# Kernel tuning notes

Hardware: AMD Instinct MI355X
Metric: run time of the kernel (lower is better)

## Reference

```python
import jax, jax.numpy as jnp
import numpy as np

B, H, P, D, NF = 16, 16, 128, 128, 12  # patches == head_dim required by lin_qk


def setup_inputs() -> dict:
    key = jax.random.key(0)
    ks = jax.random.split(key, 8)
    return {
        "q": jax.random.normal(ks[0], (B, H, P, D), jnp.float32),
        "k": jax.random.normal(ks[1], (B, H, P, D), jnp.float32),
        "scale": jnp.ones((1,), jnp.float32),  # unused by the original forward
        "grid": jnp.arange(NF, dtype=jnp.float32) + 1.0,
        "base_weight": jax.random.uniform(ks[2], (D, D), jnp.float32),
        "coef_q": jax.random.uniform(ks[3], (D, NF), jnp.float32),
        "coef_k": jax.random.uniform(ks[4], (D, NF), jnp.float32),
        "scale_base": jnp.ones((1, H, P, D), jnp.float32),
        "scale_sp": jnp.ones((1, H, P, D), jnp.float32),
        "w_qk": jax.random.normal(ks[5], (D, D), jnp.float32) / np.float32(np.sqrt(D)),
        "b_qk": jnp.zeros((D,), jnp.float32),
    }


def _branch(x, coef, grid, base_weight, scale_sp, scale_base):
    # base path: SiLU(x) @ W^T  (F.linear semantics)
    base = jax.nn.silu(x) @ base_weight.T
    # KAN sin basis: sin(grid_f * x_d) -> (B,H,P,NF,D); contract coef[d,f]
    s = jnp.sin(grid[:, None] * x[..., None, :])
    f = jnp.einsum('df,bhpfd->bhpd', coef, s)
    return jax.nn.sigmoid(f * scale_sp + base * scale_base)


def reference(q, k, scale, grid, base_weight, coef_q, coef_k, scale_base, scale_sp, w_qk, b_qk):
    # Per-channel sigmoids, then sum over D. The original builds the full
    # (B,H,P,P,D) broadcast tensor sig_q[...,p,None,:] + sig_k[...,None,p',:]
    # and sums over D; that is exactly separable:
    #   sum_d(sig_q[p,d]) + sum_d(sig_k[p',d])
    sq = _branch(q, coef_q, grid, base_weight, scale_sp, scale_base).sum(-1)  # (B,H,P)
    sk = _branch(k, coef_k, grid, base_weight, scale_sp, scale_base).sum(-1)  # (B,H,P)
    f_out = sq[..., :, None] + sk[..., None, :]  # (B,H,P,P)
    f_out = f_out @ w_qk.T + b_qk  # lin_qk: valid because patches == head_dim
    return jax.nn.softmax(f_out, axis=-1)
```

## Files before the change

kernel.cpp:

```cpp
#include <hip/hip_runtime.h>
#include <hip/hip_bf16.h>


typedef float          f32x4 __attribute__((ext_vector_type(4)));
typedef short          s16x8 __attribute__((ext_vector_type(8)));
typedef int            s32x4 __attribute__((ext_vector_type(4)));
typedef unsigned short u16x8 __attribute__((ext_vector_type(8)));

#define LOG2E   1.44269504f
#define NLOG2E -1.44269504f
#define INV2PI  0.15915494309189535f

static __device__ __forceinline__ float hw_exp2(float x) {
    float r;
    asm("v_exp_f32 %0, %1" : "=v"(r) : "v"(x));
    return r;
}
static __device__ __forceinline__ float hw_fract(float x) {
    float r;
    asm("v_fract_f32 %0, %1" : "=v"(r) : "v"(x));
    return r;
}
static __device__ __forceinline__ float hw_sin01(float f) {
    float r;
    asm("v_sin_f32 %0, %1" : "=v"(r) : "v"(f));
    return r;
}
static __device__ __forceinline__ float hw_cos01(float f) {
    float r;
    asm("v_cos_f32 %0, %1" : "=v"(r) : "v"(f));
    return r;
}
static __device__ __forceinline__ float fastrcp(float x) {
    return __builtin_amdgcn_rcpf(x);
}
static __device__ __forceinline__ unsigned int cvt_pk_bf16(float lo, float hi) {
    unsigned int r;
    asm("v_cvt_pk_bf16_f32 %0, %1, %2" : "=v"(r) : "v"(lo), "v"(hi));
    return r;
}
static __device__ __forceinline__ float sigmoid_fast(float z) {
    return fastrcp(1.f + hw_exp2(z * NLOG2E));
}
static __device__ __forceinline__ int swz(int local) {
    return local ^ (((local >> 8) & 7) << 4);
}

__global__ __launch_bounds__(256) void k_convert(const float* __restrict__ bw,
                                                 unsigned short* __restrict__ wbf) {
    int i = blockIdx.x * 256 + threadIdx.x;
    if (i < 128 * 128) {
        __hip_bfloat16 h = __float2bfloat16(bw[i]);
        unsigned short r;
        __builtin_memcpy(&r, &h, 2);
        wbf[i] = r;
    }
}

__global__ __launch_bounds__(512, 4) void k_branch(
    const float* __restrict__ q, const float* __restrict__ k,
    const unsigned short* __restrict__ wbf,
    const float* __restrict__ gridv,
    const float* __restrict__ coef_q, const float* __restrict__ coef_k,
    const float* __restrict__ sbase,
    const float* __restrict__ ssp,
    float* __restrict__ sums_lo, float* __restrict__ sums_hi)
{
    __shared__ char smem[32768 + 6144];
    float* cfl = (float*)(smem + 32768);

    const int t = threadIdx.x;
    const int lane = t & 63, w = t >> 6;
    const int wr = w >> 1;
    const int ch = w & 1;
    const int r15 = lane & 15, g4 = lane >> 4;
    const int row0 = blockIdx.x * 64;
    const bool is_q = row0 < 32768;
    const float* X = is_q ? q : k;
    const float* coef = is_q ? coef_q : coef_k;
    const int xrow0 = is_q ? row0 : row0 - 32768;
    const float g1 = gridv[0];
    const float grev = g1 * INV2PI;

    #pragma unroll
    for (int it = 0; it < 4; ++it) {
        int c = it * 512 + t;
        u16x8 v = *(const u16x8*)&wbf[c * 8];
        *(u16x8*)(smem + swz(c * 16)) = v;
    }
    #pragma unroll
    for (int it = 0; it < 3; ++it) {
        int e = it * 512 + t;
        float v = coef[e];
        int d = e / 12, u = e - d * 12;
        cfl[u * 128 + d] = v;
    }
    __syncthreads();

    const int xrow = wr * 16 + r15;
    const float* xrowp = &X[(xrow0 + xrow) * 128];
    const int hp = (row0 + xrow) & 2047;
    const float* ssprow = &ssp[hp * 128];

    f32x4 acc[4];
    #pragma unroll
    for (int n = 0; n < 4; ++n) acc[n] = (f32x4){0.f, 0.f, 0.f, 0.f};
    float fv[16];

    #pragma unroll
    for (int s = 0; s < 4; ++s) {
        const float4* xp = (const float4*)&xrowp[s * 32 + g4 * 8];
        float4 x0 = xp[0], x1 = xp[1];
        float xsv[8] = {x0.x, x0.y, x0.z, x0.w, x1.x, x1.y, x1.z, x1.w};
        float sl[8];
        #pragma unroll
        for (int j = 0; j < 8; ++j) {
            float e = hw_exp2(xsv[j] * NLOG2E);
            sl[j] = xsv[j] * fastrcp(1.f + e);
        }
        s32x4 a4 = {(int)cvt_pk_bf16(sl[0], sl[1]), (int)cvt_pk_bf16(sl[2], sl[3]),
                    (int)cvt_pk_bf16(sl[4], sl[5]), (int)cvt_pk_bf16(sl[6], sl[7])};
        s16x8 af = __builtin_bit_cast(s16x8, a4);

        if ((s >> 1) == ch) {
            const int s2 = s & 1;
            const float4* spp = (const float4*)&ssprow[s * 32 + g4 * 8];
            float4 sp0 = spp[0], sp1 = spp[1];
            float spv[8] = {sp0.x, sp0.y, sp0.z, sp0.w,
                            sp1.x, sp1.y, sp1.z, sp1.w};
            #pragma unroll
            for (int j = 0; j < 8; ++j) {
                int d = s * 32 + g4 * 8 + j;
                float rev = hw_fract(grev * xsv[j]);
                float s1 = hw_sin01(rev);
                float cv = hw_cos01(rev);
                float t2 = cv + cv;
                float sprev = 0.f, scur = s1;
                float f = cfl[d] * s1;
                #pragma unroll
                for (int u = 1; u < 12; ++u) {
                    float sn = __builtin_fmaf(t2, scur, -sprev);
                    f = __builtin_fmaf(cfl[u * 128 + d], sn, f);
                    sprev = scur; scur = sn;
                }
                fv[s2 * 8 + j] = f * spv[j];
            }
        }

        #pragma unroll
        for (int n = 0; n < 4; ++n) {
            s16x8 bfw = *(const s16x8*)(smem + swz((ch * 64 + n * 16 + r15) * 256
                                                   + s * 64 + g4 * 16));
            acc[n] = __builtin_amdgcn_mfma_f32_16x16x32_bf16(bfw, af, acc[n], 0, 0, 0);
        }
    }
    __syncthreads();

    float* myfv = (float*)smem + w * 1024;
    #pragma unroll
    for (int s2 = 0; s2 < 2; ++s2) {
        #pragma unroll
        for (int jb = 0; jb < 2; ++jb) {
            int dloc = s2 * 32 + g4 * 8 + jb * 4;
            f32x4 v = {fv[s2*8 + jb*4 + 0], fv[s2*8 + jb*4 + 1],
                       fv[s2*8 + jb*4 + 2], fv[s2*8 + jb*4 + 3]};
            *(f32x4*)&myfv[r15 * 64 + ((dloc + r15 * 4) & 63)] = v;
        }
    }

    float ps = 0.f;
    #pragma unroll
    for (int n = 0; n < 4; ++n) {
        f32x4 fp = *(f32x4*)&myfv[r15 * 64 + ((n * 16 + g4 * 4 + r15 * 4) & 63)];
        float4 sb = *(const float4*)&sbase[hp * 128 + ch * 64 + n * 16 + g4 * 4];
        float sbv[4] = {sb.x, sb.y, sb.z, sb.w};
        #pragma unroll
        for (int reg = 0; reg < 4; ++reg) {
            float z = fp[reg] + acc[n][reg] * sbv[reg];
            ps += sigmoid_fast(z);
        }
    }
    ps += __shfl_xor(ps, 16, 64);
    ps += __shfl_xor(ps, 32, 64);
    if (g4 == 0) {
        (ch ? sums_hi : sums_lo)[row0 + xrow] = ps;
    }
}

__global__ __launch_bounds__(256) void k_attn(
    const float* __restrict__ sums_lo, const float* __restrict__ sums_hi,
    const float* __restrict__ w_qk, const float* __restrict__ b_qk,
    float* __restrict__ out)
{
    __shared__ float skl[128], Tp[2][128], Rp[2][128], Tl[128], Rl[128];
    const int bh = blockIdx.x >> 1;
    const int half = blockIdx.x & 1;
    const int t = threadIdx.x;

    if (t < 128) {
        int idx = 32768 + bh * 128 + t;
        skl[t] = sums_lo[idx] + sums_hi[idx];
    }
    __syncthreads();
    {
        int j = t & 127, ph = t >> 7;
        const float4* wr = (const float4*)&w_qk[j * 128 + ph * 64];
        const float* sk2 = &skl[ph * 64];
        float a = 0.f, r = 0.f;
        #pragma unroll 8
        for (int p4 = 0; p4 < 16; ++p4) {
            float4 w4 = wr[p4];
            a += w4.x * sk2[p4 * 4 + 0] + w4.y * sk2[p4 * 4 + 1] +
                 w4.z * sk2[p4 * 4 + 2] + w4.w * sk2[p4 * 4 + 3];
            r += w4.x + w4.y + w4.z + w4.w;
        }
        Tp[ph][j] = a;
        Rp[ph][j] = r;
    }
    __syncthreads();
    if (t < 128) {
        Tl[t] = Tp[0][t] + Tp[1][t] + b_qk[t];
        Rl[t] = Rp[0][t] + Rp[1][t];
    }
    __syncthreads();

    const int lane = t & 63, w = t >> 6;
    #pragma unroll
    for (int it = 0; it < 16; ++it) {
        int row = bh * 128 + half * 64 + it * 4 + w;
        float sqv = sums_lo[row] + sums_hi[row];
        float2 r2 = *(const float2*)&Rl[lane * 2];
        float2 t2 = *(const float2*)&Tl[lane * 2];
        float l0 = __builtin_fmaf(sqv, r2.x, t2.x);
        float l1 = __builtin_fmaf(sqv, r2.y, t2.y);
        float m = fmaxf(l0, l1);
        #pragma unroll
        for (int s = 32; s >= 1; s >>= 1) m = fmaxf(m, __shfl_xor(m, s, 64));
        float e0 = hw_exp2((l0 - m) * LOG2E);
        float e1 = hw_exp2((l1 - m) * LOG2E);
        float sum = e0 + e1;
        #pragma unroll
        for (int w2 = 32; w2 >= 1; w2 >>= 1) sum += __shfl_xor(sum, w2, 64);
        float inv = fastrcp(sum);
        float2 o2 = {e0 * inv, e1 * inv};
        *(float2*)&out[row * 128 + lane * 2] = o2;
    }
}

extern "C" void kernel_launch(void* const* d_in, const int* in_sizes, int n_in,
                              void* d_out, int out_size, void* d_ws, size_t ws_size,
                              hipStream_t stream) {
    (void)in_sizes; (void)n_in; (void)out_size; (void)ws_size;
    const float* q      = (const float*)d_in[0];
    const float* k      = (const float*)d_in[1];
    const float* gridv  = (const float*)d_in[3];
    const float* bw     = (const float*)d_in[4];
    const float* coef_q = (const float*)d_in[5];
    const float* coef_k = (const float*)d_in[6];
    const float* sbase  = (const float*)d_in[7];
    const float* ssp    = (const float*)d_in[8];
    const float* w_qk   = (const float*)d_in[9];
    const float* b_qk   = (const float*)d_in[10];

    float* out  = (float*)d_out;
    float* ws      = (float*)d_ws;
    float* sums_lo = ws;
    float* sums_hi = ws + 65536;
    unsigned short* wbf = (unsigned short*)(ws + 131072);

    k_convert<<<64, 256, 0, stream>>>(bw, wbf);
    k_branch<<<1024, 512, 0, stream>>>(q, k, wbf, gridv, coef_q, coef_k,
                                       sbase, ssp, sums_lo, sums_hi);
    k_attn<<<512, 256, 0, stream>>>(sums_lo, sums_hi, w_qk, b_qk, out);
}
```

Baseline: 41.05 us.

## Fuse weight conversion into branch kernel, pack sin recurrence, halve attn grid

Removes the separate bf16 conversion kernel: each branch block now reads the fp32 base weight and converts it to bf16 while filling shared memory, saving one launch at the cost of redundant conversion in every block. The Chebyshev-style sin recurrence is rewritten to process two channels at once with packed v_pk_fma/v_pk_mul instructions to cut VALU instruction count. The attention kernel now handles a full 128-row head per block instead of half, which halves the redundant per-block w_qk reductions but also halves the grid.

```diff
diff --git a/kernel.cpp b/kernel.cpp
--- a/kernel.cpp
+++ b/kernel.cpp
@@ -3,9 +3,10 @@
 
 
 typedef float          f32x4 __attribute__((ext_vector_type(4)));
+typedef float          f32x2 __attribute__((ext_vector_type(2)));
 typedef short          s16x8 __attribute__((ext_vector_type(8)));
 typedef int            s32x4 __attribute__((ext_vector_type(4)));
-typedef unsigned short u16x8 __attribute__((ext_vector_type(8)));
+typedef unsigned int   u32x4 __attribute__((ext_vector_type(4)));
 
 #define LOG2E   1.44269504f
 #define NLOG2E -1.44269504f
@@ -42,24 +43,29 @@
 static __device__ __forceinline__ float sigmoid_fast(float z) {
     return fastrcp(1.f + hw_exp2(z * NLOG2E));
 }
+static __device__ __forceinline__ f32x2 pk_mul(f32x2 a, f32x2 b) {
+    f32x2 d;
+    asm("v_pk_mul_f32 %0, %1, %2" : "=v"(d) : "v"(a), "v"(b));
+    return d;
+}
+static __device__ __forceinline__ f32x2 pk_fma(f32x2 a, f32x2 b, f32x2 c) {
+    f32x2 d;
+    asm("v_pk_fma_f32 %0, %1, %2, %3" : "=v"(d) : "v"(a), "v"(b), "v"(c));
+    return d;
+}
+static __device__ __forceinline__ f32x2 pk_fma_nc(f32x2 a, f32x2 b, f32x2 c) {
+    f32x2 d;
+    asm("v_pk_fma_f32 %0, %1, %2, %3 neg_lo:[0,0,1] neg_hi:[0,0,1]"
+        : "=v"(d) : "v"(a), "v"(b), "v"(c));
+    return d;
+}
 static __device__ __forceinline__ int swz(int local) {
     return local ^ (((local >> 8) & 7) << 4);
 }
 
-__global__ __launch_bounds__(256) void k_convert(const float* __restrict__ bw,
-                                                 unsigned short* __restrict__ wbf) {
-    int i = blockIdx.x * 256 + threadIdx.x;
-    if (i < 128 * 128) {
-        __hip_bfloat16 h = __float2bfloat16(bw[i]);
-        unsigned short r;
-        __builtin_memcpy(&r, &h, 2);
-        wbf[i] = r;
-    }
-}
-
 __global__ __launch_bounds__(512, 4) void k_branch(
     const float* __restrict__ q, const float* __restrict__ k,
-    const unsigned short* __restrict__ wbf,
+    const float* __restrict__ bw,
     const float* __restrict__ gridv,
     const float* __restrict__ coef_q, const float* __restrict__ coef_k,
     const float* __restrict__ sbase,
@@ -85,8 +91,11 @@
     #pragma unroll
     for (int it = 0; it < 4; ++it) {
         int c = it * 512 + t;
-        u16x8 v = *(const u16x8*)&wbf[c * 8];
-        *(u16x8*)(smem + swz(c * 16)) = v;
+        const float4* wp = (const float4*)&bw[(c >> 4) * 128 + (c & 15) * 8];
+        float4 w0 = wp[0], w1 = wp[1];
+        u32x4 v = {cvt_pk_bf16(w0.x, w0.y), cvt_pk_bf16(w0.z, w0.w),
+                   cvt_pk_bf16(w1.x, w1.y), cvt_pk_bf16(w1.z, w1.w)};
+        *(u32x4*)(smem + swz(c * 16)) = v;
     }
     #pragma unroll
     for (int it = 0; it < 3; ++it) {
@@ -129,21 +138,28 @@
             float spv[8] = {sp0.x, sp0.y, sp0.z, sp0.w,
                             sp1.x, sp1.y, sp1.z, sp1.w};
             #pragma unroll
-            for (int j = 0; j < 8; ++j) {
-                int d = s * 32 + g4 * 8 + j;
-                float rev = hw_fract(grev * xsv[j]);
-                float s1 = hw_sin01(rev);
-                float cv = hw_cos01(rev);
-                float t2 = cv + cv;
-                float sprev = 0.f, scur = s1;
-                float f = cfl[d] * s1;
+            for (int j2 = 0; j2 < 4; ++j2) {
+                int d = s * 32 + g4 * 8 + j2 * 2;
+                float xa = xsv[j2 * 2], xb = xsv[j2 * 2 + 1];
+                float ra = hw_fract(grev * xa), rb = hw_fract(grev * xb);
+                float sa = hw_sin01(ra), sb = hw_sin01(rb);
+                float ca = hw_cos01(ra), cb = hw_cos01(rb);
+                f32x2 t2p = {ca + ca, cb + cb};
+                f32x2 scur = {sa, sb};
+                f32x2 sprev = scur;
+                f32x2 f2 = pk_mul(*(const f32x2*)&cfl[d], scur);
+                scur = pk_mul(t2p, scur);
+                f2 = pk_fma(*(const f32x2*)&cfl[128 + d], scur, f2);
                 #pragma unroll
-                for (int u = 1; u < 12; ++u) {
-                    float sn = __builtin_fmaf(t2, scur, -sprev);
-                    f = __builtin_fmaf(cfl[u * 128 + d], sn, f);
+                for (int u = 2; u < 12; ++u) {
+                    f32x2 sn = pk_fma_nc(t2p, scur, sprev);
+                    f2 = pk_fma(*(const f32x2*)&cfl[u * 128 + d], sn, f2);
                     sprev = scur; scur = sn;
                 }
-                fv[s2 * 8 + j] = f * spv[j];
+                f32x2 sp2 = {spv[j2 * 2], spv[j2 * 2 + 1]};
+                f32x2 r = pk_mul(f2, sp2);
+                fv[s2 * 8 + j2 * 2]     = r[0];
+                fv[s2 * 8 + j2 * 2 + 1] = r[1];
             }
         }
 
@@ -193,8 +209,7 @@
     float* __restrict__ out)
 {
     __shared__ float skl[128], Tp[2][128], Rp[2][128], Tl[128], Rl[128];
-    const int bh = blockIdx.x >> 1;
-    const int half = blockIdx.x & 1;
+    const int bh = blockIdx.x;
     const int t = threadIdx.x;
 
     if (t < 128) {
@@ -225,9 +240,9 @@
     __syncthreads();
 
     const int lane = t & 63, w = t >> 6;
-    #pragma unroll
-    for (int it = 0; it < 16; ++it) {
-        int row = bh * 128 + half * 64 + it * 4 + w;
+    #pragma unroll 8
+    for (int it = 0; it < 32; ++it) {
+        int row = bh * 128 + it * 4 + w;
         float sqv = sums_lo[row] + sums_hi[row];
         float2 r2 = *(const float2*)&Rl[lane * 2];
         float2 t2 = *(const float2*)&Tl[lane * 2];
@@ -266,10 +281,8 @@
     float* ws      = (float*)d_ws;
     float* sums_lo = ws;
     float* sums_hi = ws + 65536;
-    unsigned short* wbf = (unsigned short*)(ws + 131072);
-
-    k_convert<<<64, 256, 0, stream>>>(bw, wbf);
-    k_branch<<<1024, 512, 0, stream>>>(q, k, wbf, gridv, coef_q, coef_k,
+
+    k_branch<<<1024, 512, 0, stream>>>(q, k, bw, gridv, coef_q, coef_k,
                                        sbase, ssp, sums_lo, sums_hi);
-    k_attn<<<512, 256, 0, stream>>>(sums_lo, sums_hi, w_qk, b_qk, out);
-}
+    k_attn<<<256, 256, 0, stream>>>(sums_lo, sums_hi, w_qk, b_qk, out);
+}
```

New measurement: 38.36 us. 1.07x faster.
